# Kernel tuning notes

Measured on AMD Instinct MI355X. Metric: run time of the kernel, lower is better.

## Reference

```python
import jax, jax.numpy as jnp
import numpy as np

B, Z, A = 1024, 512, 8          # batch_size, z_dim, action_dim
AH, ZH = 64, 512                # action_hidden_dim, z_hidden_dim
N_NEG = 100                     # n_neg_actions
TEMP = 0.1                      # temperature
TOP_K = (1, 3, 10)


def forward_model(z, a, Wa, ba, W1, b1, W2, b2):
    # MLP forward model with skip connection (z_delta=True):
    # embed action, concat with z, 2-layer MLP predicting a delta.
    h_a = jax.nn.relu(a @ Wa + ba)                                   # [..., AH]
    h = jax.nn.relu(jnp.concatenate([jnp.broadcast_to(z, a.shape[:-1] + (Z,)), h_a], axis=-1) @ W1 + b1)  # [..., ZH]
    delta = h @ W2 + b2                                              # [..., Z]
    return z + delta


def setup_inputs() -> dict:
    key = jax.random.key(0)
    ks = jax.random.split(key, 8)
    def w(k, shape, fan_in):
        return jax.random.normal(k, shape, jnp.float32) / np.float32(np.sqrt(fan_in))
    z = jax.random.normal(ks[0], (B, Z), jnp.float32)
    z_next = jax.random.normal(ks[1], (B, Z), jnp.float32)
    z_next_hat = jax.random.normal(ks[2], (B, Z), jnp.float32)
    actions = jax.random.normal(ks[3], (B, A), jnp.float32)
    Wa = w(ks[4], (A, AH), A)
    ba = jnp.zeros((AH,), jnp.float32)
    W1 = w(ks[5], (Z + AH, ZH), Z + AH)
    b1 = jnp.zeros((ZH,), jnp.float32)
    W2 = w(ks[6], (ZH, Z), ZH)
    b2 = jnp.zeros((Z,), jnp.float32)
    return {"z": z, "z_next": z_next, "z_next_hat": z_next_hat, "actions": actions,
            "Wa": Wa, "ba": ba, "W1": W1, "b1": b1, "W2": W2, "b2": b2}


def reference(z, z_next, z_next_hat, actions, Wa, ba, W1, b1, W2, b2):
    # ControlCPC.compute_loss with dot_product_similarity, vectorized:
    # the Python loop over n_neg_actions rolled-action forward-model calls
    # becomes one batched [n-1, B, ...] forward-model evaluation.
    batch = z.shape[0]
    n = min(N_NEG, batch)
    sim = z_next @ z_next_hat.T                                      # [B, B] positives on diagonal
    shifts = jnp.arange(1, n)
    neg_actions = jax.vmap(lambda i: jnp.roll(actions, -i, axis=0))(shifts)  # [n-1, B, A]
    z_hat_neg = forward_model(z[None], neg_actions, Wa, ba, W1, b1, W2, b2)  # [n-1, B, Z]
    neg_sim = jnp.einsum('nbz,bz->bn', z_hat_neg, z_next)            # diag of similarity per shift
    sim_mat = jnp.concatenate([sim, neg_sim], axis=1)                # [B, B+n-1]
    # INCE loss, positives on diagonal
    logp = jax.nn.log_softmax(sim_mat / jnp.float32(TEMP), axis=1)
    loss = -jnp.mean(jnp.diagonal(logp))                             # diagonal takes first B entries
    labels = jnp.arange(batch)[:, None]
    accs = []
    for k in TOP_K:
        _, preds = jax.lax.top_k(sim_mat, k)                         # [B, k]
        accs.append(jnp.mean((preds == labels).astype(jnp.float32)) * k)
    return (loss, accs[0], accs[1], accs[2])
```

## Files before the change

kernel.cpp:

```cpp
#include <hip/hip_runtime.h>
#include <math.h>

#define B_SZ 1024
#define Z_DIM 512
#define A_DIM 8
#define AH 64
#define ZH 512
#define NNEG 99
#define INV_T 10.0f

typedef __attribute__((ext_vector_type(8))) short short8;
typedef __attribute__((ext_vector_type(4))) float f32x4;

__device__ __forceinline__ short bf16rn(float x) {
    unsigned u = __float_as_uint(x);
    u += 0x7fffu + ((u >> 16) & 1u);
    return (short)(u >> 16);
}
__device__ __forceinline__ void cvt8rn(float4 x0, float4 x1, short8& h) {
    h[0] = bf16rn(x0.x); h[1] = bf16rn(x0.y); h[2] = bf16rn(x0.z); h[3] = bf16rn(x0.w);
    h[4] = bf16rn(x1.x); h[5] = bf16rn(x1.y); h[6] = bf16rn(x1.z); h[7] = bf16rn(x1.w);
}

__device__ __forceinline__ int sw(int m, int kb) { return m * 8 + (kb ^ (m & 7)); }

__global__ __launch_bounds__(256) void prep_kernel(
    const float* __restrict__ W1, const float* __restrict__ actions,
    const float* __restrict__ Wa, const float* __restrict__ ba,
    float* __restrict__ W1T, float* __restrict__ ha, unsigned* __restrict__ cnt)
{
    const int id = blockIdx.x, tid = threadIdx.x;
    if (id == 0 && tid == 0) atomicExch(cnt, 0u);
    if (id < 72) {
        __shared__ float L[64][68];
        int kt = id >> 3, nt = id & 7;
#pragma unroll
        for (int i = 0; i < 4; ++i) {
            int f = tid + i * 256;
            int r = f >> 4, c4 = (f & 15) << 2;
            *(float4*)&L[r][c4] = *(const float4*)&W1[(kt * 64 + r) * 512 + nt * 64 + c4];
        }
        __syncthreads();
#pragma unroll
        for (int i = 0; i < 4; ++i) {
            int f = tid + i * 256;
            int r = f >> 4, c4 = (f & 15) << 2;
            float4 o = {L[c4][r], L[c4 + 1][r], L[c4 + 2][r], L[c4 + 3][r]};
            *(float4*)&W1T[(nt * 64 + r) * 576 + kt * 64 + c4] = o;
        }
    } else if (id < 88) {
        __shared__ float sWa[A_DIM * 64];
        __shared__ float sba[64];
        __shared__ float sact[64][A_DIM];
        int j0 = (id - 72) * 64;
        for (int i = tid; i < A_DIM * 64; i += 256) sWa[i] = Wa[i];
        if (tid < 64) sba[tid] = ba[tid];
        for (int i = tid; i < 64 * A_DIM; i += 256) (&sact[0][0])[i] = actions[j0 * A_DIM + i];
        __syncthreads();
        int r = tid >> 2, c0 = (tid & 3) * 16;
        float o[16];
#pragma unroll
        for (int c = 0; c < 16; ++c) o[c] = sba[c0 + c];
#pragma unroll
        for (int k = 0; k < A_DIM; ++k) {
            float a = sact[r][k];
#pragma unroll
            for (int c = 0; c < 16; ++c) o[c] += a * sWa[k * 64 + c0 + c];
        }
#pragma unroll
        for (int c = 0; c < 16; c += 4) {
            float4 v4 = {fmaxf(o[c], 0.f), fmaxf(o[c + 1], 0.f),
                         fmaxf(o[c + 2], 0.f), fmaxf(o[c + 3], 0.f)};
            *(float4*)&ha[(j0 + r) * 64 + c0 + c] = v4;
        }
    }
}

__global__ __launch_bounds__(256) void mm_kernel(
    const float* __restrict__ z, const float* __restrict__ z_next,
    const float* __restrict__ z_next_hat, const float* __restrict__ W1T,
    const float* __restrict__ b1, const float* __restrict__ W2,
    const float* __restrict__ ha,
    float* __restrict__ sim, float* __restrict__ u, float* __restrict__ v,
    float* __restrict__ g)
{
    __shared__ short Ah[4096], Bh[4096];

    const int id = blockIdx.x;
    const int tid = threadIdx.x;

    const float* Aop; const float* Bop; const float* bias = nullptr;
    float* C; int N, K, lda, ldb, bm0, bn0;
    if (id < 256) {
        int t = id; bn0 = (t & 15) * 64; bm0 = (t >> 4) * 64;
        Aop = z_next; lda = 512; Bop = z_next_hat; ldb = 512;
        C = sim; N = 1024; K = 512;
    } else if (id < 384) {
        int t = id - 256; bn0 = (t & 7) * 64; bm0 = (t >> 3) * 64;
        Aop = z; lda = 512; Bop = W1T; ldb = 576;
        C = u; N = 512; K = 512; bias = b1;
    } else if (id < 512) {
        int t = id - 384; bn0 = (t & 7) * 64; bm0 = (t >> 3) * 64;
        Aop = z_next; lda = 512; Bop = W2; ldb = 512;
        C = v; N = 512; K = 512;
    } else {
        int t = id - 512; bn0 = (t & 7) * 64; bm0 = (t >> 3) * 64;
        Aop = ha; lda = 64; Bop = W1T + 512; ldb = 576;
        C = g; N = 512; K = 64;
    }

    const int lane = tid & 63, wv = tid >> 6;
    const int lm = lane & 15, lq = lane >> 4;
    const int wm = (wv >> 1) * 32, wn = (wv & 1) * 32;
    const int sr = tid >> 2, sq = tid & 3;
    short8* Ah8 = (short8*)Ah; short8* Bh8 = (short8*)Bh;
    f32x4 acc[2][2] = {};

    for (int k0 = 0; k0 < K; k0 += 64) {
        {
            const float* base = &Aop[(bm0 + sr) * lda + k0 + sq * 16];
            float4 x0 = *(const float4*)(base + 0), x1 = *(const float4*)(base + 4);
            float4 x2 = *(const float4*)(base + 8), x3 = *(const float4*)(base + 12);
            short8 h;
            cvt8rn(x0, x1, h); Ah8[sw(sr, 2 * sq)] = h;
            cvt8rn(x2, x3, h); Ah8[sw(sr, 2 * sq + 1)] = h;
        }
        {
            const float* base = &Bop[(bn0 + sr) * ldb + k0 + sq * 16];
            float4 x0 = *(const float4*)(base + 0), x1 = *(const float4*)(base + 4);
            float4 x2 = *(const float4*)(base + 8), x3 = *(const float4*)(base + 12);
            short8 h;
            cvt8rn(x0, x1, h); Bh8[sw(sr, 2 * sq)] = h;
            cvt8rn(x2, x3, h); Bh8[sw(sr, 2 * sq + 1)] = h;
        }
        __syncthreads();
#pragma unroll
        for (int kk = 0; kk < 64; kk += 32) {
            int kbi = (kk >> 3) + lq;
            short8 ah[2], bh[2];
#pragma unroll
            for (int i = 0; i < 2; ++i) {
                ah[i] = Ah8[sw(wm + i * 16 + lm, kbi)];
                bh[i] = Bh8[sw(wn + i * 16 + lm, kbi)];
            }
#pragma unroll
            for (int i = 0; i < 2; ++i)
#pragma unroll
                for (int j = 0; j < 2; ++j)
                    acc[i][j] = __builtin_amdgcn_mfma_f32_16x16x32_bf16(ah[i], bh[j], acc[i][j], 0, 0, 0);
        }
        __syncthreads();
    }
#pragma unroll
    for (int i = 0; i < 2; ++i)
#pragma unroll
        for (int j = 0; j < 2; ++j) {
            int n = bn0 + wn + j * 16 + lm;
            float bb = bias ? bias[n] : 0.0f;
#pragma unroll
            for (int r = 0; r < 4; ++r) {
                int m = bm0 + wm + i * 16 + lq * 4 + r;
                C[m * N + n] = acc[i][j][r] + bb;
            }
        }
}

__global__ __launch_bounds__(256) void row2_kernel(
    const float* __restrict__ sim, const float* __restrict__ u,
    const float* __restrict__ v, const float* __restrict__ g,
    const float* __restrict__ z, const float* __restrict__ z_next,
    const float* __restrict__ b2,
    float* __restrict__ pw, unsigned* __restrict__ cnt, float* __restrict__ out)
{
    const int blk = blockIdx.x;
    const int tid = threadIdx.x;
    const int w = tid >> 6, lane = tid & 63;
    const int b = blk * 4 + w;
    __shared__ float gbuf[8][512];
    __shared__ float rn[4][100];
    __shared__ float sacc[4][4];
    __shared__ float red[256];
    __shared__ int sdone;

    float4 ua = *(const float4*)&u[b * 512 + lane * 4];
    float4 ub = *(const float4*)&u[b * 512 + 256 + lane * 4];
    float4 va = *(const float4*)&v[b * 512 + lane * 4];
    float4 vb = *(const float4*)&v[b * 512 + 256 + lane * 4];

    float p;
    {
        float4 za = *(const float4*)&z[b * 512 + lane * 4];
        float4 zb = *(const float4*)&z[b * 512 + 256 + lane * 4];
        float4 na = *(const float4*)&z_next[b * 512 + lane * 4];
        float4 nb = *(const float4*)&z_next[b * 512 + 256 + lane * 4];
        float4 ca = *(const float4*)&b2[lane * 4];
        float4 cb = *(const float4*)&b2[256 + lane * 4];
        p  = (za.x + ca.x) * na.x + (za.y + ca.y) * na.y + (za.z + ca.z) * na.z + (za.w + ca.w) * na.w;
        p += (zb.x + cb.x) * nb.x + (zb.y + cb.y) * nb.y + (zb.z + cb.z) * nb.z + (zb.w + cb.w) * nb.w;
    }
    for (int off = 32; off; off >>= 1) p += __shfl_down(p, off);
    const float c0 = __shfl(p, 0);

    const int J0 = blk * 4;
    for (int it = 0; it < 13; ++it) {
#pragma unroll
        for (int ph = 0; ph < 4; ++ph) {
            int f4i = tid + ph * 256;
            int row = f4i >> 7, c = f4i & 127;
            int idx = it * 8 + row;
            if (idx < 102) {
                int jr = (J0 + 1 + idx) & (B_SZ - 1);
                *(float4*)&gbuf[row][c * 4] = *(const float4*)&g[jr * 512 + c * 4];
            }
        }
        __syncthreads();
        float d[8];
#pragma unroll
        for (int ri = 0; ri < 8; ++ri) {
            float4 g0 = *(const float4*)&gbuf[ri][lane * 4];
            float4 g1 = *(const float4*)&gbuf[ri][256 + lane * 4];
            float t = 0.0f;
            t += fmaxf(ua.x + g0.x, 0.0f) * va.x;
            t += fmaxf(ua.y + g0.y, 0.0f) * va.y;
            t += fmaxf(ua.z + g0.z, 0.0f) * va.z;
            t += fmaxf(ua.w + g0.w, 0.0f) * va.w;
            t += fmaxf(ub.x + g1.x, 0.0f) * vb.x;
            t += fmaxf(ub.y + g1.y, 0.0f) * vb.y;
            t += fmaxf(ub.z + g1.z, 0.0f) * vb.z;
            t += fmaxf(ub.w + g1.w, 0.0f) * vb.w;
            d[ri] = t;
        }
        for (int off = 32; off; off >>= 1) {
#pragma unroll
            for (int ri = 0; ri < 8; ++ri) d[ri] += __shfl_down(d[ri], off);
        }
        if (lane == 0) {
#pragma unroll
            for (int ri = 0; ri < 8; ++ri) {
                int idx = it * 8 + ri;
                int s1 = idx - w;
                if (idx < 102 && s1 >= 0 && s1 < 99) rn[w][s1] = c0 + d[ri];
            }
        }
        __syncthreads();
    }

    float4 sv[4];
#pragma unroll
    for (int i = 0; i < 4; ++i)
        sv[i] = *(const float4*)&sim[b * 1024 + lane * 16 + i * 4];
    float nva = rn[w][lane];
    float nvb = (lane < 35) ? rn[w][lane + 64] : -3.4e38f;
    float diag = sim[b * 1024 + b];

    float m = fmaxf(nva, nvb);
#pragma unroll
    for (int i = 0; i < 4; ++i)
        m = fmaxf(m, fmaxf(fmaxf(sv[i].x, sv[i].y), fmaxf(sv[i].z, sv[i].w)));
    for (int off = 32; off; off >>= 1) m = fmaxf(m, __shfl_xor(m, off));

    float es = 0.0f; int ck = 0;
#pragma unroll
    for (int i = 0; i < 4; ++i) {
        float xs[4] = {sv[i].x, sv[i].y, sv[i].z, sv[i].w};
#pragma unroll
        for (int c = 0; c < 4; ++c) {
            int j = lane * 16 + i * 4 + c;
            float x = xs[c];
            es += __expf((x - m) * INV_T);
            if (x > diag) ck++;
            else if (j < b && x == diag) ck++;
        }
    }
    es += __expf((nva - m) * INV_T);
    if (nva > diag) ck++;
    if (lane < 35) {
        es += __expf((nvb - m) * INV_T);
        if (nvb > diag) ck++;
    }
    for (int off = 32; off; off >>= 1) {
        es += __shfl_down(es, off);
        ck += __shfl_down(ck, off);
    }
    if (lane == 0) {
        float loss_b = (m - diag) * INV_T + logf(es);
        sacc[w][0] = loss_b;
        sacc[w][1] = (ck < 1) ? 1.0f : 0.0f;
        sacc[w][2] = (ck < 3) ? 1.0f : 0.0f;
        sacc[w][3] = (ck < 10) ? 1.0f : 0.0f;
    }
    __syncthreads();
    if (tid == 0) {
#pragma unroll
        for (int c = 0; c < 4; ++c)
            pw[blk * 4 + c] = sacc[0][c] + sacc[1][c] + sacc[2][c] + sacc[3][c];
        __threadfence();
        unsigned old = atomicAdd(cnt, 1u);
        sdone = (old == 255u) ? 1 : 0;
    }
    __syncthreads();
    if (sdone) {
        __threadfence();
        int c = tid & 3;
        float s = 0.0f;
        for (int r = tid >> 2; r < 256; r += 64) s += pw[r * 4 + c];
        red[tid] = s;
        __syncthreads();
        if (tid < 4) {
            float t = 0.0f;
            for (int q = 0; q < 64; ++q) t += red[tid + q * 4];
            out[tid] = t * (1.0f / (float)B_SZ);
        }
    }
}

extern "C" void kernel_launch(void* const* d_in, const int* in_sizes, int n_in,
                              void* d_out, int out_size, void* d_ws, size_t ws_size,
                              hipStream_t stream) {
    const float* z          = (const float*)d_in[0];
    const float* z_next     = (const float*)d_in[1];
    const float* z_next_hat = (const float*)d_in[2];
    const float* actions    = (const float*)d_in[3];
    const float* Wa         = (const float*)d_in[4];
    const float* ba         = (const float*)d_in[5];
    const float* W1         = (const float*)d_in[6];
    const float* b1         = (const float*)d_in[7];
    const float* W2         = (const float*)d_in[8];
    const float* b2         = (const float*)d_in[9];
    float* out = (float*)d_out;

    float* ws   = (float*)d_ws;
    float* sim  = ws;
    float* u    = sim + B_SZ * B_SZ;
    float* v    = u + B_SZ * ZH;
    float* g    = v + B_SZ * ZH;
    float* W1T  = g + B_SZ * ZH;
    float* ha   = W1T + 512 * 576;
    float* pw   = ha + B_SZ * AH;
    unsigned* cnt = (unsigned*)(pw + 256 * 4);

    prep_kernel<<<88, 256, 0, stream>>>(W1, actions, Wa, ba, W1T, ha, cnt);
    mm_kernel<<<640, 256, 0, stream>>>(z, z_next, z_next_hat, W1T, b1, W2, ha,
                                       sim, u, v, g);
    row2_kernel<<<256, 256, 0, stream>>>(sim, u, v, g, z, z_next, b2, pw, cnt, out);
}
```

Before: 121.6 us.

## Assign one row per block and split negatives across warps in row2 kernel

The final row kernel now runs one batch row per 256-thread block (1024 blocks) instead of four rows per block. The four warps each compute about 25 of the 99 negative-shift similarities, loading g rows straight from global memory into registers instead of staging them through a shared buffer with a barrier per iteration. The softmax and rank statistics are then reduced across the whole block. This raises parallelism and removes the per-iteration barriers, at the cost of cross-warp reductions and four times as many per-row partials for the last block to sum.

```diff
diff --git a/kernel.cpp b/kernel.cpp
--- a/kernel.cpp
+++ b/kernel.cpp
@@ -172,13 +172,11 @@
     const float* __restrict__ b2,
     float* __restrict__ pw, unsigned* __restrict__ cnt, float* __restrict__ out)
 {
-    const int blk = blockIdx.x;
+    const int b = blockIdx.x;
     const int tid = threadIdx.x;
     const int w = tid >> 6, lane = tid & 63;
-    const int b = blk * 4 + w;
-    __shared__ float gbuf[8][512];
-    __shared__ float rn[4][100];
-    __shared__ float sacc[4][4];
+    __shared__ float rn[100];
+    __shared__ float sred[12];
     __shared__ float red[256];
     __shared__ int sdone;
 
@@ -201,109 +199,99 @@
     for (int off = 32; off; off >>= 1) p += __shfl_down(p, off);
     const float c0 = __shfl(p, 0);
 
-    const int J0 = blk * 4;
-    for (int it = 0; it < 13; ++it) {
-#pragma unroll
-        for (int ph = 0; ph < 4; ++ph) {
-            int f4i = tid + ph * 256;
-            int row = f4i >> 7, c = f4i & 127;
-            int idx = it * 8 + row;
-            if (idx < 102) {
-                int jr = (J0 + 1 + idx) & (B_SZ - 1);
-                *(float4*)&gbuf[row][c * 4] = *(const float4*)&g[jr * 512 + c * 4];
+    const int base = w * 25;
+    const int cntw = (w < 3) ? 25 : 24;
+#pragma unroll
+    for (int rr = 0; rr < 4; ++rr) {
+        float4 ga[8], gb[8];
+        float t[8];
+#pragma unroll
+        for (int c = 0; c < 8; ++c) {
+            int q = rr * 8 + c;
+            if (q < cntw) {
+                int j = (b + 1 + base + q) & (B_SZ - 1);
+                ga[c] = *(const float4*)&g[j * 512 + lane * 4];
+                gb[c] = *(const float4*)&g[j * 512 + 256 + lane * 4];
             }
         }
-        __syncthreads();
-        float d[8];
-#pragma unroll
-        for (int ri = 0; ri < 8; ++ri) {
-            float4 g0 = *(const float4*)&gbuf[ri][lane * 4];
-            float4 g1 = *(const float4*)&gbuf[ri][256 + lane * 4];
-            float t = 0.0f;
-            t += fmaxf(ua.x + g0.x, 0.0f) * va.x;
-            t += fmaxf(ua.y + g0.y, 0.0f) * va.y;
-            t += fmaxf(ua.z + g0.z, 0.0f) * va.z;
-            t += fmaxf(ua.w + g0.w, 0.0f) * va.w;
-            t += fmaxf(ub.x + g1.x, 0.0f) * vb.x;
-            t += fmaxf(ub.y + g1.y, 0.0f) * vb.y;
-            t += fmaxf(ub.z + g1.z, 0.0f) * vb.z;
-            t += fmaxf(ub.w + g1.w, 0.0f) * vb.w;
-            d[ri] = t;
+#pragma unroll
+        for (int c = 0; c < 8; ++c) {
+            float s = 0.0f;
+            s += fmaxf(ua.x + ga[c].x, 0.0f) * va.x;
+            s += fmaxf(ua.y + ga[c].y, 0.0f) * va.y;
+            s += fmaxf(ua.z + ga[c].z, 0.0f) * va.z;
+            s += fmaxf(ua.w + ga[c].w, 0.0f) * va.w;
+            s += fmaxf(ub.x + gb[c].x, 0.0f) * vb.x;
+            s += fmaxf(ub.y + gb[c].y, 0.0f) * vb.y;
+            s += fmaxf(ub.z + gb[c].z, 0.0f) * vb.z;
+            s += fmaxf(ub.w + gb[c].w, 0.0f) * vb.w;
+            t[c] = s;
         }
         for (int off = 32; off; off >>= 1) {
 #pragma unroll
-            for (int ri = 0; ri < 8; ++ri) d[ri] += __shfl_down(d[ri], off);
+            for (int c = 0; c < 8; ++c) t[c] += __shfl_down(t[c], off);
         }
         if (lane == 0) {
 #pragma unroll
-            for (int ri = 0; ri < 8; ++ri) {
-                int idx = it * 8 + ri;
-                int s1 = idx - w;
-                if (idx < 102 && s1 >= 0 && s1 < 99) rn[w][s1] = c0 + d[ri];
+            for (int c = 0; c < 8; ++c) {
+                int q = rr * 8 + c;
+                if (q < cntw) rn[base + q] = c0 + t[c];
             }
         }
-        __syncthreads();
-    }
-
-    float4 sv[4];
-#pragma unroll
-    for (int i = 0; i < 4; ++i)
-        sv[i] = *(const float4*)&sim[b * 1024 + lane * 16 + i * 4];
-    float nva = rn[w][lane];
-    float nvb = (lane < 35) ? rn[w][lane + 64] : -3.4e38f;
+    }
+    __syncthreads();
+
+    float4 s4 = *(const float4*)&sim[b * 1024 + tid * 4];
+    float neg = (tid < NNEG) ? rn[tid] : -3.4e38f;
     float diag = sim[b * 1024 + b];
 
-    float m = fmaxf(nva, nvb);
-#pragma unroll
-    for (int i = 0; i < 4; ++i)
-        m = fmaxf(m, fmaxf(fmaxf(sv[i].x, sv[i].y), fmaxf(sv[i].z, sv[i].w)));
+    float m = fmaxf(fmaxf(s4.x, s4.y), fmaxf(s4.z, s4.w));
+    m = fmaxf(m, neg);
     for (int off = 32; off; off >>= 1) m = fmaxf(m, __shfl_xor(m, off));
+    if (lane == 0) sred[w] = m;
+    __syncthreads();
+    m = fmaxf(fmaxf(sred[0], sred[1]), fmaxf(sred[2], sred[3]));
 
     float es = 0.0f; int ck = 0;
-#pragma unroll
-    for (int i = 0; i < 4; ++i) {
-        float xs[4] = {sv[i].x, sv[i].y, sv[i].z, sv[i].w};
+    {
+        float xs[4] = {s4.x, s4.y, s4.z, s4.w};
 #pragma unroll
         for (int c = 0; c < 4; ++c) {
-            int j = lane * 16 + i * 4 + c;
+            int j = tid * 4 + c;
             float x = xs[c];
             es += __expf((x - m) * INV_T);
             if (x > diag) ck++;
             else if (j < b && x == diag) ck++;
         }
     }
-    es += __expf((nva - m) * INV_T);
-    if (nva > diag) ck++;
-    if (lane < 35) {
-        es += __expf((nvb - m) * INV_T);
-        if (nvb > diag) ck++;
-    }
+    if (tid < NNEG) {
+        es += __expf((neg - m) * INV_T);
+        if (neg > diag) ck++;
+    }
+    float ckf = (float)ck;
     for (int off = 32; off; off >>= 1) {
         es += __shfl_down(es, off);
-        ck += __shfl_down(ck, off);
-    }
-    if (lane == 0) {
-        float loss_b = (m - diag) * INV_T + logf(es);
-        sacc[w][0] = loss_b;
-        sacc[w][1] = (ck < 1) ? 1.0f : 0.0f;
-        sacc[w][2] = (ck < 3) ? 1.0f : 0.0f;
-        sacc[w][3] = (ck < 10) ? 1.0f : 0.0f;
-    }
+        ckf += __shfl_down(ckf, off);
+    }
+    if (lane == 0) { sred[4 + w] = es; sred[8 + w] = ckf; }
     __syncthreads();
     if (tid == 0) {
-#pragma unroll
-        for (int c = 0; c < 4; ++c)
-            pw[blk * 4 + c] = sacc[0][c] + sacc[1][c] + sacc[2][c] + sacc[3][c];
+        float est = sred[4] + sred[5] + sred[6] + sred[7];
+        int ckt = (int)(sred[8] + sred[9] + sred[10] + sred[11]);
+        pw[b * 4 + 0] = (m - diag) * INV_T + logf(est);
+        pw[b * 4 + 1] = (ckt < 1) ? 1.0f : 0.0f;
+        pw[b * 4 + 2] = (ckt < 3) ? 1.0f : 0.0f;
+        pw[b * 4 + 3] = (ckt < 10) ? 1.0f : 0.0f;
         __threadfence();
         unsigned old = atomicAdd(cnt, 1u);
-        sdone = (old == 255u) ? 1 : 0;
+        sdone = (old == 1023u) ? 1 : 0;
     }
     __syncthreads();
     if (sdone) {
         __threadfence();
         int c = tid & 3;
         float s = 0.0f;
-        for (int r = tid >> 2; r < 256; r += 64) s += pw[r * 4 + c];
+        for (int r = tid >> 2; r < 1024; r += 64) s += pw[r * 4 + c];
         red[tid] = s;
         __syncthreads();
         if (tid < 4) {
@@ -337,10 +325,10 @@
     float* W1T  = g + B_SZ * ZH;
     float* ha   = W1T + 512 * 576;
     float* pw   = ha + B_SZ * AH;
-    unsigned* cnt = (unsigned*)(pw + 256 * 4);
+    unsigned* cnt = (unsigned*)(pw + B_SZ * 4);
 
     prep_kernel<<<88, 256, 0, stream>>>(W1, actions, Wa, ba, W1T, ha, cnt);
     mm_kernel<<<640, 256, 0, stream>>>(z, z_next, z_next_hat, W1T, b1, W2, ha,
                                        sim, u, v, g);
-    row2_kernel<<<256, 256, 0, stream>>>(sim, u, v, g, z, z_next, b2, pw, cnt, out);
-}
+    row2_kernel<<<1024, 256, 0, stream>>>(sim, u, v, g, z, z_next, b2, pw, cnt, out);
+}
```

Result: slower. 129.8 us (+6.7%).

## Fold prep kernel into GEMM and double-buffer g rows via async LDS loads

Applied to the files above, without the earlier changes.

Removes the separate prep kernel. The W1 transpose is replaced by reading W1 row-major and scattering it into the swizzled LDS B tile, and the action embedding is computed inside the GEMM blocks that use it. The row kernel now stages g rows with global_load_lds into a double buffer using manual vmcnt waits and raw barriers, which overlaps loads with the relu-dot compute. The atomic last-block reduction is replaced by a tiny final kernel, adding one launch and a scattered 2-byte LDS store pattern for the B tile.

```diff
diff --git a/kernel.cpp b/kernel.cpp
--- a/kernel.cpp
+++ b/kernel.cpp
@@ -24,89 +24,48 @@
 
 __device__ __forceinline__ int sw(int m, int kb) { return m * 8 + (kb ^ (m & 7)); }
 
-__global__ __launch_bounds__(256) void prep_kernel(
-    const float* __restrict__ W1, const float* __restrict__ actions,
-    const float* __restrict__ Wa, const float* __restrict__ ba,
-    float* __restrict__ W1T, float* __restrict__ ha, unsigned* __restrict__ cnt)
-{
-    const int id = blockIdx.x, tid = threadIdx.x;
-    if (id == 0 && tid == 0) atomicExch(cnt, 0u);
-    if (id < 72) {
-        __shared__ float L[64][68];
-        int kt = id >> 3, nt = id & 7;
-#pragma unroll
-        for (int i = 0; i < 4; ++i) {
-            int f = tid + i * 256;
-            int r = f >> 4, c4 = (f & 15) << 2;
-            *(float4*)&L[r][c4] = *(const float4*)&W1[(kt * 64 + r) * 512 + nt * 64 + c4];
-        }
-        __syncthreads();
-#pragma unroll
-        for (int i = 0; i < 4; ++i) {
-            int f = tid + i * 256;
-            int r = f >> 4, c4 = (f & 15) << 2;
-            float4 o = {L[c4][r], L[c4 + 1][r], L[c4 + 2][r], L[c4 + 3][r]};
-            *(float4*)&W1T[(nt * 64 + r) * 576 + kt * 64 + c4] = o;
-        }
-    } else if (id < 88) {
-        __shared__ float sWa[A_DIM * 64];
-        __shared__ float sba[64];
-        __shared__ float sact[64][A_DIM];
-        int j0 = (id - 72) * 64;
-        for (int i = tid; i < A_DIM * 64; i += 256) sWa[i] = Wa[i];
-        if (tid < 64) sba[tid] = ba[tid];
-        for (int i = tid; i < 64 * A_DIM; i += 256) (&sact[0][0])[i] = actions[j0 * A_DIM + i];
-        __syncthreads();
-        int r = tid >> 2, c0 = (tid & 3) * 16;
-        float o[16];
-#pragma unroll
-        for (int c = 0; c < 16; ++c) o[c] = sba[c0 + c];
-#pragma unroll
-        for (int k = 0; k < A_DIM; ++k) {
-            float a = sact[r][k];
-#pragma unroll
-            for (int c = 0; c < 16; ++c) o[c] += a * sWa[k * 64 + c0 + c];
-        }
-#pragma unroll
-        for (int c = 0; c < 16; c += 4) {
-            float4 v4 = {fmaxf(o[c], 0.f), fmaxf(o[c + 1], 0.f),
-                         fmaxf(o[c + 2], 0.f), fmaxf(o[c + 3], 0.f)};
-            *(float4*)&ha[(j0 + r) * 64 + c0 + c] = v4;
-        }
-    }
+#define VMWAIT(N) asm volatile("s_waitcnt vmcnt(" #N ")" ::: "memory")
+__device__ __forceinline__ void raw_barrier() {
+    asm volatile("" ::: "memory");
+    __builtin_amdgcn_s_barrier();
+    asm volatile("" ::: "memory");
+}
+typedef const __attribute__((address_space(1))) void* gas_ptr;
+typedef __attribute__((address_space(3))) void* las_ptr;
+__device__ __forceinline__ void gld_lds16(const float* gsrc, float* ldst) {
+    __builtin_amdgcn_global_load_lds((gas_ptr)gsrc, (las_ptr)ldst, 16, 0, 0);
 }
 
 __global__ __launch_bounds__(256) void mm_kernel(
     const float* __restrict__ z, const float* __restrict__ z_next,
-    const float* __restrict__ z_next_hat, const float* __restrict__ W1T,
+    const float* __restrict__ z_next_hat, const float* __restrict__ W1,
     const float* __restrict__ b1, const float* __restrict__ W2,
-    const float* __restrict__ ha,
+    const float* __restrict__ actions, const float* __restrict__ Wa,
+    const float* __restrict__ ba,
     float* __restrict__ sim, float* __restrict__ u, float* __restrict__ v,
     float* __restrict__ g)
 {
     __shared__ short Ah[4096], Bh[4096];
+    __shared__ float sWa[A_DIM * 64];
+    __shared__ float sba[64];
 
     const int id = blockIdx.x;
     const int tid = threadIdx.x;
 
-    const float* Aop; const float* Bop; const float* bias = nullptr;
-    float* C; int N, K, lda, ldb, bm0, bn0;
+    const float* Aop = nullptr; const float* Bsrc; const float* bias = nullptr;
+    float* C; int N, K, bm0, bn0, mode;
     if (id < 256) {
         int t = id; bn0 = (t & 15) * 64; bm0 = (t >> 4) * 64;
-        Aop = z_next; lda = 512; Bop = z_next_hat; ldb = 512;
-        C = sim; N = 1024; K = 512;
+        Aop = z_next; Bsrc = z_next_hat; C = sim; N = 1024; K = 512; mode = 0;
     } else if (id < 384) {
         int t = id - 256; bn0 = (t & 7) * 64; bm0 = (t >> 3) * 64;
-        Aop = z; lda = 512; Bop = W1T; ldb = 576;
-        C = u; N = 512; K = 512; bias = b1;
+        Aop = z; Bsrc = W1; C = u; N = 512; K = 512; bias = b1; mode = 1;
     } else if (id < 512) {
         int t = id - 384; bn0 = (t & 7) * 64; bm0 = (t >> 3) * 64;
-        Aop = z_next; lda = 512; Bop = W2; ldb = 512;
-        C = v; N = 512; K = 512;
+        Aop = z_next; Bsrc = W2; C = v; N = 512; K = 512; mode = 0;
     } else {
         int t = id - 512; bn0 = (t & 7) * 64; bm0 = (t >> 3) * 64;
-        Aop = ha; lda = 64; Bop = W1T + 512; ldb = 576;
-        C = g; N = 512; K = 64;
+        Bsrc = W1 + 512 * 512; C = g; N = 512; K = 64; mode = 2;
     }
 
     const int lane = tid & 63, wv = tid >> 6;
@@ -116,22 +75,59 @@
     short8* Ah8 = (short8*)Ah; short8* Bh8 = (short8*)Bh;
     f32x4 acc[2][2] = {};
 
+    float aA[16];
+    if (mode == 2) {
+        for (int i = tid; i < A_DIM * 64; i += 256) sWa[i] = Wa[i];
+        if (tid < 64) sba[tid] = ba[tid];
+        __syncthreads();
+        float4 a0 = *(const float4*)&actions[(bm0 + sr) * A_DIM + 0];
+        float4 a1 = *(const float4*)&actions[(bm0 + sr) * A_DIM + 4];
+        float av[8] = {a0.x, a0.y, a0.z, a0.w, a1.x, a1.y, a1.z, a1.w};
+#pragma unroll
+        for (int c = 0; c < 16; ++c) aA[c] = sba[sq * 16 + c];
+#pragma unroll
+        for (int k = 0; k < A_DIM; ++k)
+#pragma unroll
+            for (int c = 0; c < 16; ++c) aA[c] += av[k] * sWa[k * 64 + sq * 16 + c];
+#pragma unroll
+        for (int c = 0; c < 16; ++c) aA[c] = fmaxf(aA[c], 0.0f);
+    }
+
     for (int k0 = 0; k0 < K; k0 += 64) {
-        {
-            const float* base = &Aop[(bm0 + sr) * lda + k0 + sq * 16];
+        if (mode != 2) {
+            const float* base = &Aop[(bm0 + sr) * 512 + k0 + sq * 16];
             float4 x0 = *(const float4*)(base + 0), x1 = *(const float4*)(base + 4);
             float4 x2 = *(const float4*)(base + 8), x3 = *(const float4*)(base + 12);
             short8 h;
             cvt8rn(x0, x1, h); Ah8[sw(sr, 2 * sq)] = h;
             cvt8rn(x2, x3, h); Ah8[sw(sr, 2 * sq + 1)] = h;
-        }
-        {
-            const float* base = &Bop[(bn0 + sr) * ldb + k0 + sq * 16];
+        } else {
+            short8 h;
+#pragma unroll
+            for (int c = 0; c < 8; ++c) h[c] = bf16rn(aA[c]);
+            Ah8[sw(sr, 2 * sq)] = h;
+#pragma unroll
+            for (int c = 0; c < 8; ++c) h[c] = bf16rn(aA[8 + c]);
+            Ah8[sw(sr, 2 * sq + 1)] = h;
+        }
+        if (mode == 0) {
+            const float* base = &Bsrc[(bn0 + sr) * 512 + k0 + sq * 16];
             float4 x0 = *(const float4*)(base + 0), x1 = *(const float4*)(base + 4);
             float4 x2 = *(const float4*)(base + 8), x3 = *(const float4*)(base + 12);
             short8 h;
             cvt8rn(x0, x1, h); Bh8[sw(sr, 2 * sq)] = h;
             cvt8rn(x2, x3, h); Bh8[sw(sr, 2 * sq + 1)] = h;
+        } else {
+            const float* base = &Bsrc[(k0 + sr) * 512 + bn0 + sq * 16];
+            float4 x0 = *(const float4*)(base + 0), x1 = *(const float4*)(base + 4);
+            float4 x2 = *(const float4*)(base + 8), x3 = *(const float4*)(base + 12);
+            float xs[16] = {x0.x, x0.y, x0.z, x0.w, x1.x, x1.y, x1.z, x1.w,
+                            x2.x, x2.y, x2.z, x2.w, x3.x, x3.y, x3.z, x3.w};
+            short* Bs = (short*)Bh;
+            int kb = sr >> 3, ke = sr & 7;
+#pragma unroll
+            for (int t = 0; t < 16; ++t)
+                Bs[sw(sq * 16 + t, kb) * 8 + ke] = bf16rn(xs[t]);
         }
         __syncthreads();
 #pragma unroll
@@ -170,22 +166,37 @@
     const float* __restrict__ v, const float* __restrict__ g,
     const float* __restrict__ z, const float* __restrict__ z_next,
     const float* __restrict__ b2,
-    float* __restrict__ pw, unsigned* __restrict__ cnt, float* __restrict__ out)
+    float* __restrict__ pw)
 {
     const int blk = blockIdx.x;
     const int tid = threadIdx.x;
     const int w = tid >> 6, lane = tid & 63;
     const int b = blk * 4 + w;
-    __shared__ float gbuf[8][512];
+    __shared__ float gbuf[2][8][512];
     __shared__ float rn[4][100];
-    __shared__ float sacc[4][4];
-    __shared__ float red[256];
-    __shared__ int sdone;
+
+    const int J0 = blk * 4;
+
+    auto STAGE = [&](int c, int bi) {
+        int i0 = c * 8 + 2 * w, i1 = i0 + 1;
+        int j0 = (J0 + 1 + i0) & (B_SZ - 1);
+        int j1 = (J0 + 1 + i1) & (B_SZ - 1);
+        gld_lds16(&g[j0 * 512 + lane * 4],       &gbuf[bi][2 * w][0]);
+        gld_lds16(&g[j0 * 512 + 256 + lane * 4], &gbuf[bi][2 * w][256]);
+        gld_lds16(&g[j1 * 512 + lane * 4],       &gbuf[bi][2 * w + 1][0]);
+        gld_lds16(&g[j1 * 512 + 256 + lane * 4], &gbuf[bi][2 * w + 1][256]);
+    };
+    STAGE(0, 0);
 
     float4 ua = *(const float4*)&u[b * 512 + lane * 4];
     float4 ub = *(const float4*)&u[b * 512 + 256 + lane * 4];
     float4 va = *(const float4*)&v[b * 512 + lane * 4];
     float4 vb = *(const float4*)&v[b * 512 + 256 + lane * 4];
+    float4 sv[4];
+#pragma unroll
+    for (int i = 0; i < 4; ++i)
+        sv[i] = *(const float4*)&sim[b * 1024 + lane * 16 + i * 4];
+    float diag = sim[b * 1024 + b];
 
     float p;
     {
@@ -201,24 +212,16 @@
     for (int off = 32; off; off >>= 1) p += __shfl_down(p, off);
     const float c0 = __shfl(p, 0);
 
-    const int J0 = blk * 4;
-    for (int it = 0; it < 13; ++it) {
-#pragma unroll
-        for (int ph = 0; ph < 4; ++ph) {
-            int f4i = tid + ph * 256;
-            int row = f4i >> 7, c = f4i & 127;
-            int idx = it * 8 + row;
-            if (idx < 102) {
-                int jr = (J0 + 1 + idx) & (B_SZ - 1);
-                *(float4*)&gbuf[row][c * 4] = *(const float4*)&g[jr * 512 + c * 4];
-            }
-        }
-        __syncthreads();
+    for (int c = 0; c < 12; ++c) {
+        const int bi = c & 1, bn2 = bi ^ 1;
+        STAGE(c + 1, bn2);
+        VMWAIT(4);
+        raw_barrier();
         float d[8];
 #pragma unroll
         for (int ri = 0; ri < 8; ++ri) {
-            float4 g0 = *(const float4*)&gbuf[ri][lane * 4];
-            float4 g1 = *(const float4*)&gbuf[ri][256 + lane * 4];
+            float4 g0 = *(const float4*)&gbuf[bi][ri][lane * 4];
+            float4 g1 = *(const float4*)&gbuf[bi][ri][256 + lane * 4];
             float t = 0.0f;
             t += fmaxf(ua.x + g0.x, 0.0f) * va.x;
             t += fmaxf(ua.y + g0.y, 0.0f) * va.y;
@@ -237,21 +240,47 @@
         if (lane == 0) {
 #pragma unroll
             for (int ri = 0; ri < 8; ++ri) {
-                int idx = it * 8 + ri;
-                int s1 = idx - w;
-                if (idx < 102 && s1 >= 0 && s1 < 99) rn[w][s1] = c0 + d[ri];
+                int s1 = c * 8 + ri - w;
+                if (s1 >= 0 && s1 < NNEG) rn[w][s1] = c0 + d[ri];
             }
         }
-        __syncthreads();
-    }
-
-    float4 sv[4];
-#pragma unroll
-    for (int i = 0; i < 4; ++i)
-        sv[i] = *(const float4*)&sim[b * 1024 + lane * 16 + i * 4];
+        raw_barrier();
+    }
+    VMWAIT(0);
+    raw_barrier();
+    {
+        float d[8];
+#pragma unroll
+        for (int ri = 0; ri < 8; ++ri) {
+            float4 g0 = *(const float4*)&gbuf[0][ri][lane * 4];
+            float4 g1 = *(const float4*)&gbuf[0][ri][256 + lane * 4];
+            float t = 0.0f;
+            t += fmaxf(ua.x + g0.x, 0.0f) * va.x;
+            t += fmaxf(ua.y + g0.y, 0.0f) * va.y;
+            t += fmaxf(ua.z + g0.z, 0.0f) * va.z;
+            t += fmaxf(ua.w + g0.w, 0.0f) * va.w;
+            t += fmaxf(ub.x + g1.x, 0.0f) * vb.x;
+            t += fmaxf(ub.y + g1.y, 0.0f) * vb.y;
+            t += fmaxf(ub.z + g1.z, 0.0f) * vb.z;
+            t += fmaxf(ub.w + g1.w, 0.0f) * vb.w;
+            d[ri] = t;
+        }
+        for (int off = 32; off; off >>= 1) {
+#pragma unroll
+            for (int ri = 0; ri < 8; ++ri) d[ri] += __shfl_down(d[ri], off);
+        }
+        if (lane == 0) {
+#pragma unroll
+            for (int ri = 0; ri < 8; ++ri) {
+                int s1 = 96 + ri - w;
+                if (s1 >= 0 && s1 < NNEG) rn[w][s1] = c0 + d[ri];
+            }
+        }
+    }
+    __syncthreads();
+
     float nva = rn[w][lane];
     float nvb = (lane < 35) ? rn[w][lane + 64] : -3.4e38f;
-    float diag = sim[b * 1024 + b];
 
     float m = fmaxf(nva, nvb);
 #pragma unroll
@@ -283,34 +312,27 @@
         ck += __shfl_down(ck, off);
     }
     if (lane == 0) {
-        float loss_b = (m - diag) * INV_T + logf(es);
-        sacc[w][0] = loss_b;
-        sacc[w][1] = (ck < 1) ? 1.0f : 0.0f;
-        sacc[w][2] = (ck < 3) ? 1.0f : 0.0f;
-        sacc[w][3] = (ck < 10) ? 1.0f : 0.0f;
-    }
+        pw[b * 4 + 0] = (m - diag) * INV_T + logf(es);
+        pw[b * 4 + 1] = (ck < 1) ? 1.0f : 0.0f;
+        pw[b * 4 + 2] = (ck < 3) ? 1.0f : 0.0f;
+        pw[b * 4 + 3] = (ck < 10) ? 1.0f : 0.0f;
+    }
+}
+
+__global__ __launch_bounds__(256) void final_kernel(
+    const float* __restrict__ pw, float* __restrict__ out)
+{
+    __shared__ float red[256];
+    const int tid = threadIdx.x;
+    const int c = tid & 3;
+    float s = 0.0f;
+    for (int r = tid >> 2; r < 1024; r += 64) s += pw[r * 4 + c];
+    red[tid] = s;
     __syncthreads();
-    if (tid == 0) {
-#pragma unroll
-        for (int c = 0; c < 4; ++c)
-            pw[blk * 4 + c] = sacc[0][c] + sacc[1][c] + sacc[2][c] + sacc[3][c];
-        __threadfence();
-        unsigned old = atomicAdd(cnt, 1u);
-        sdone = (old == 255u) ? 1 : 0;
-    }
-    __syncthreads();
-    if (sdone) {
-        __threadfence();
-        int c = tid & 3;
-        float s = 0.0f;
-        for (int r = tid >> 2; r < 256; r += 64) s += pw[r * 4 + c];
-        red[tid] = s;
-        __syncthreads();
-        if (tid < 4) {
-            float t = 0.0f;
-            for (int q = 0; q < 64; ++q) t += red[tid + q * 4];
-            out[tid] = t * (1.0f / (float)B_SZ);
-        }
+    if (tid < 4) {
+        float t = 0.0f;
+        for (int q = 0; q < 64; ++q) t += red[tid + q * 4];
+        out[tid] = t * (1.0f / (float)B_SZ);
     }
 }
 
@@ -334,13 +356,10 @@
     float* u    = sim + B_SZ * B_SZ;
     float* v    = u + B_SZ * ZH;
     float* g    = v + B_SZ * ZH;
-    float* W1T  = g + B_SZ * ZH;
-    float* ha   = W1T + 512 * 576;
-    float* pw   = ha + B_SZ * AH;
-    unsigned* cnt = (unsigned*)(pw + 256 * 4);
-
-    prep_kernel<<<88, 256, 0, stream>>>(W1, actions, Wa, ba, W1T, ha, cnt);
-    mm_kernel<<<640, 256, 0, stream>>>(z, z_next, z_next_hat, W1T, b1, W2, ha,
-                                       sim, u, v, g);
-    row2_kernel<<<256, 256, 0, stream>>>(sim, u, v, g, z, z_next, b2, pw, cnt, out);
-}
+    float* pw   = g + B_SZ * ZH;
+
+    mm_kernel<<<640, 256, 0, stream>>>(z, z_next, z_next_hat, W1, b1, W2,
+                                       actions, Wa, ba, sim, u, v, g);
+    row2_kernel<<<256, 256, 0, stream>>>(sim, u, v, g, z, z_next, b2, pw);
+    final_kernel<<<1, 256, 0, stream>>>(pw, out);
+}
```

Result: faster. 118.9 us (-2.2%).
